# Kernel optimization log

Hardware: AMD Instinct MI355X
Metric: run time of the kernel (lower is better)

Reference implementation:

```python
import jax, jax.numpy as jnp
import numpy as np

B, T, IN_DIM = 32, 1024, 32
E, H, P = 256, 4, 32  # embed_dim, heads, max_patches
HD = E // H


def _lin(x, w, b):
    # torch nn.Linear: y = x @ W.T + b, W: [out, in]
    return jnp.einsum('...i,oi->...o', x, w) + b


def setup_inputs() -> dict:
    key = jax.random.key(0)
    ks = jax.random.split(key, 13)
    s = 0.02
    return {
        'x': jax.random.normal(ks[0], (B, T, IN_DIM), jnp.float32),
        'ip_w': jax.random.normal(ks[1], (E, IN_DIM), jnp.float32) * s,
        'ip_b': jnp.zeros((E,), jnp.float32),
        'in_proj_w': jax.random.normal(ks[2], (3 * E, E), jnp.float32) * s,
        'in_proj_b': jnp.zeros((3 * E,), jnp.float32),
        'out_w': jax.random.normal(ks[3], (E, E), jnp.float32) * s,
        'out_b': jnp.zeros((E,), jnp.float32),
        'bp_w1': jax.random.normal(ks[4], (32, E), jnp.float32) * s,
        'bp_b1': jnp.zeros((32,), jnp.float32),
        'bp_w2': jax.random.normal(ks[5], (1, 32), jnp.float32) * s,
        'bp_b2': jnp.zeros((1,), jnp.float32),
        'pr_w': jax.random.normal(ks[6], (E, E), jnp.float32) * s,
        'pr_b': jnp.zeros((E,), jnp.float32),
    }


def reference(x, ip_w, ip_b, in_proj_w, in_proj_b, out_w, out_b,
              bp_w1, bp_b1, bp_w2, bp_b2, pr_w, pr_b):
    # input projection
    h = _lin(x, ip_w, ip_b)  # [B,T,E]
    # MultiheadAttention (self-attn, batch_first, eval/no-dropout)
    qkv = _lin(h, in_proj_w, in_proj_b)  # [B,T,3E]
    q, k, v = jnp.split(qkv, 3, axis=-1)
    q = q.reshape(B, T, H, HD)
    k = k.reshape(B, T, H, HD)
    v = v.reshape(B, T, H, HD)
    scores = jnp.einsum('bqhd,bkhd->bhqk', q, k) / jnp.sqrt(jnp.float32(HD))
    attn = jax.nn.softmax(scores, axis=-1)
    ctx = jnp.einsum('bhqk,bkhd->bqhd', attn, v).reshape(B, T, E)
    attn_out = _lin(ctx, out_w, out_b)  # [B,T,E]
    # boundary scores
    bscore = jax.nn.sigmoid(_lin(jax.nn.relu(_lin(attn_out, bp_w1, bp_b1)), bp_w2, bp_b2))[..., 0]  # [B,T]
    cbp = jnp.cumsum(bscore, axis=1)
    cbp = cbp / (cbp[:, -1:] + 1e-6)
    pid = jnp.minimum(jnp.floor(cbp * P).astype(jnp.int32), P - 1)  # [B,T]
    # segment-mean pooling via scatter-add
    b_idx = jnp.broadcast_to(jnp.arange(B)[:, None], (B, T))
    pe = jnp.zeros((B, P, E), attn_out.dtype).at[b_idx, pid].add(attn_out)
    cnt = jnp.zeros((B, P), attn_out.dtype).at[b_idx, pid].add(1.0)
    pe = pe / jnp.clip(cnt, 1.0)[..., None]
    return _lin(pe, pr_w, pr_b)  # [B,P,E]
```

## Files before the change

### kernel.cpp

```cpp
#include <hip/hip_runtime.h>
#include <math.h>

constexpr int Bn  = 32;
constexpr int Tn  = 1024;
constexpr int INn = 32;
constexpr int En  = 256;
constexpr int Pn  = 32;

typedef short bf16x8 __attribute__((ext_vector_type(8)));
typedef float f32x4  __attribute__((ext_vector_type(4)));

__device__ __forceinline__ unsigned short f2bf(float f) {
    unsigned int b = __float_as_uint(f);
    b += 0x7FFF + ((b >> 16) & 1);
    return (unsigned short)(b >> 16);
}
__device__ __forceinline__ float bf2f(unsigned short h) {
    return __uint_as_float(((unsigned int)h) << 16);
}

__global__ __launch_bounds__(256) void k_prep(const float* __restrict__ ipw,
                                              const float* __restrict__ ipb,
                                              const float* __restrict__ inw,
                                              const float* __restrict__ inb,
                                              const float* __restrict__ outw,
                                              const float* __restrict__ w1,
                                              unsigned short* __restrict__ Wcb,
                                              float* __restrict__ bc,
                                              unsigned short* __restrict__ Wb,
                                              unsigned short* __restrict__ w1h,
                                              unsigned short* __restrict__ w1l) {
    int blk = blockIdx.x, tid = threadIdx.x;
    if (blk < 96) {
        int idx = blk * 256 + tid;
        int o = idx >> 5, i = idx & 31;
        const float* wr = inw + (size_t)o * En;
        float a0 = 0.f, a1 = 0.f;
        for (int e = 0; e < En; e += 2) {
            a0 += wr[e]     * ipw[(size_t)e * INn + i];
            a1 += wr[e + 1] * ipw[(size_t)(e + 1) * INn + i];
        }
        Wcb[(size_t)o * INn + i] = f2bf(a0 + a1);
    } else if (blk < 99) {
        int o = (blk - 96) * 256 + tid;
        const float* wr = inw + (size_t)o * En;
        float a = inb[o];
        for (int e = 0; e < En; ++e) a += wr[e] * ipb[e];
        bc[o] = a;
    } else if (blk < 163) {
        int idx = (blk - 99) * 256 + tid;
        float4 a = *(const float4*)(outw + (size_t)idx * 4);
        unsigned int u0 = f2bf(a.x) | ((unsigned int)f2bf(a.y) << 16);
        unsigned int u1 = f2bf(a.z) | ((unsigned int)f2bf(a.w) << 16);
        *(uint2*)(Wb + (size_t)idx * 4) = make_uint2(u0, u1);
    } else {
        int idx = (blk - 163) * 256 + tid;
        float a = w1[idx];
        unsigned short h = f2bf(a);
        w1h[idx] = h;
        w1l[idx] = f2bf(a - bf2f(h));
    }
}

__global__ __launch_bounds__(256, 2) void k_qkv(const float* __restrict__ x,
                                                const unsigned short* __restrict__ Wcb,
                                                const float* __restrict__ bc,
                                                unsigned short* __restrict__ Qb,
                                                unsigned short* __restrict__ Kb,
                                                unsigned short* __restrict__ Vt) {
    int tid = threadIdx.x;
    int wv = tid >> 6, lane = tid & 63;
    int cl = lane & 15, quad = lane >> 4;
    int m0 = blockIdx.x * 64;
    int b = m0 >> 10, tl0 = m0 & 1023;
    int n0w = wv * 192;
    f32x4 zero4 = {0.f, 0.f, 0.f, 0.f};

    bf16x8 wfrag[12]; float bv[12];
#pragma unroll
    for (int nt = 0; nt < 12; ++nt) {
        int col = n0w + nt * 16 + cl;
        wfrag[nt] = *(const bf16x8*)(Wcb + (size_t)col * 32 + quad * 8);
        bv[nt] = bc[col];
    }
#pragma unroll
    for (int mt = 0; mt < 4; ++mt) {
        const float* xr = x + (size_t)(m0 + mt * 16 + cl) * 32 + quad * 8;
        float4 xa = *(const float4*)xr, xc = *(const float4*)(xr + 4);
        bf16x8 af;
        af[0] = (short)f2bf(xa.x); af[1] = (short)f2bf(xa.y);
        af[2] = (short)f2bf(xa.z); af[3] = (short)f2bf(xa.w);
        af[4] = (short)f2bf(xc.x); af[5] = (short)f2bf(xc.y);
        af[6] = (short)f2bf(xc.z); af[7] = (short)f2bf(xc.w);
        f32x4 acc[12];
#pragma unroll
        for (int nt = 0; nt < 12; ++nt)
            acc[nt] = __builtin_amdgcn_mfma_f32_16x16x32_bf16(af, wfrag[nt], zero4, 0, 0, 0);
        int tloc = tl0 + mt * 16 + quad * 4;
#pragma unroll
        for (int nt = 0; nt < 12; ++nt) {
            int col = n0w + nt * 16 + cl;
            int slot = col >> 8, c = col & 255;
            int h = c >> 6, d = c & 63;
            int bh = b * 4 + h;
            if (slot == 2) {
                unsigned int u0 = f2bf(acc[nt][0] + bv[nt]) |
                                  ((unsigned int)f2bf(acc[nt][1] + bv[nt]) << 16);
                unsigned int u1 = f2bf(acc[nt][2] + bv[nt]) |
                                  ((unsigned int)f2bf(acc[nt][3] + bv[nt]) << 16);
                *(uint2*)(Vt + ((size_t)bh * 64 + d) * 1024 + tloc) = make_uint2(u0, u1);
            } else {
                unsigned short* dst = (slot ? Kb : Qb) +
                                      ((size_t)bh * 1024 + tloc) * 64 + d;
#pragma unroll
                for (int r = 0; r < 4; ++r)
                    dst[(size_t)r * 64] = f2bf(acc[nt][r] + bv[nt]);
            }
        }
    }
}

__global__ __launch_bounds__(256, 4) void k_attn(const unsigned short* __restrict__ Qb,
                                                 const unsigned short* __restrict__ Kb,
                                                 const unsigned short* __restrict__ Vt,
                                                 unsigned short* __restrict__ Po0,
                                                 unsigned short* __restrict__ Po1,
                                                 float* __restrict__ L0,
                                                 float* __restrict__ L1) {
    __shared__ unsigned short Ks[64][72];
    __shared__ unsigned short Vs[64][72];
    __shared__ __align__(16) unsigned short Pl[4][2][16][40];
    int blk = blockIdx.x;
    int bh = blk & 127;
    int r_ = blk >> 7;
    int qb = r_ & 7, half = r_ >> 3;
    int b = bh >> 2, h = bh & 3;
    int tid = threadIdx.x;
    int wv = tid >> 6, lane = tid & 63;
    int cl = lane & 15, quad = lane >> 4;
    int qbase = qb * 128 + wv * 32;

    f32x4 zero4 = {0.f, 0.f, 0.f, 0.f};
    bf16x8 qfrag[2][2];
#pragma unroll
    for (int tt = 0; tt < 2; ++tt)
#pragma unroll
        for (int ch = 0; ch < 2; ++ch)
            qfrag[tt][ch] = *(const bf16x8*)(Qb +
                ((size_t)bh * 1024 + qbase + tt * 16 + cl) * 64 + ch * 32 + quad * 8);
    f32x4 acc[2][4];
#pragma unroll
    for (int tt = 0; tt < 2; ++tt)
#pragma unroll
        for (int dt = 0; dt < 4; ++dt) acc[tt][dt] = zero4;
    float l[2] = {0.f, 0.f};

    const unsigned short* Kbase = Kb + (size_t)bh * 65536;
    const unsigned short* Vbase = Vt + (size_t)bh * 65536;

    for (int kt = 0; kt < 8; ++kt) {
        int ktt = half * 8 + kt;
#pragma unroll
        for (int r = 0; r < 2; ++r) {
            int idx = r * 256 + tid; int row = idx >> 3, c16 = idx & 7;
            *(uint4*)&Ks[row][c16 * 8] =
                *(const uint4*)(Kbase + (size_t)(ktt * 64 + row) * 64 + c16 * 8);
            *(uint4*)&Vs[row][c16 * 8] =
                *(const uint4*)(Vbase + (size_t)row * 1024 + ktt * 64 + c16 * 8);
        }
        __syncthreads();
#pragma unroll
        for (int c = 0; c < 2; ++c) {
            bf16x8 ka0 = *(const bf16x8*)&Ks[c * 32 + cl][quad * 8];
            bf16x8 ka1 = *(const bf16x8*)&Ks[c * 32 + cl][32 + quad * 8];
            bf16x8 kb0 = *(const bf16x8*)&Ks[c * 32 + 16 + cl][quad * 8];
            bf16x8 kb1 = *(const bf16x8*)&Ks[c * 32 + 16 + cl][32 + quad * 8];
            bf16x8 va[4];
#pragma unroll
            for (int dt = 0; dt < 4; ++dt)
                va[dt] = *(const bf16x8*)&Vs[dt * 16 + cl][c * 32 + quad * 8];
#pragma unroll
            for (int tt = 0; tt < 2; ++tt) {
                f32x4 s0 = __builtin_amdgcn_mfma_f32_16x16x32_bf16(ka0, qfrag[tt][0], zero4, 0, 0, 0);
                s0 = __builtin_amdgcn_mfma_f32_16x16x32_bf16(ka1, qfrag[tt][1], s0, 0, 0, 0);
                f32x4 s1 = __builtin_amdgcn_mfma_f32_16x16x32_bf16(kb0, qfrag[tt][0], zero4, 0, 0, 0);
                s1 = __builtin_amdgcn_mfma_f32_16x16x32_bf16(kb1, qfrag[tt][1], s1, 0, 0, 0);
                float p0 = __expf(0.125f * s0[0]), p1 = __expf(0.125f * s0[1]);
                float p2 = __expf(0.125f * s0[2]), p3 = __expf(0.125f * s0[3]);
                float p4 = __expf(0.125f * s1[0]), p5 = __expf(0.125f * s1[1]);
                float p6 = __expf(0.125f * s1[2]), p7 = __expf(0.125f * s1[3]);
                l[tt] += ((p0 + p1) + (p2 + p3)) + ((p4 + p5) + (p6 + p7));
                unsigned int w0 = f2bf(p0) | ((unsigned int)f2bf(p1) << 16);
                unsigned int w1 = f2bf(p2) | ((unsigned int)f2bf(p3) << 16);
                unsigned int w2 = f2bf(p4) | ((unsigned int)f2bf(p5) << 16);
                unsigned int w3 = f2bf(p6) | ((unsigned int)f2bf(p7) << 16);
                *(uint2*)&Pl[wv][tt][cl][quad * 4]      = make_uint2(w0, w1);
                *(uint2*)&Pl[wv][tt][cl][16 + quad * 4] = make_uint2(w2, w3);
            }
            asm volatile("s_waitcnt lgkmcnt(0)" ::: "memory");
#pragma unroll
            for (int tt = 0; tt < 2; ++tt) {
                bf16x8 pf = *(const bf16x8*)&Pl[wv][tt][cl][quad * 8];
#pragma unroll
                for (int dt = 0; dt < 4; ++dt)
                    acc[tt][dt] = __builtin_amdgcn_mfma_f32_16x16x32_bf16(pf, va[dt], acc[tt][dt], 0, 0, 0);
            }
        }
        __syncthreads();
    }
#pragma unroll
    for (int tt = 0; tt < 2; ++tt) {
        l[tt] += __shfl_xor(l[tt], 16);
        l[tt] += __shfl_xor(l[tt], 32);
    }
    unsigned short* Po = half ? Po1 : Po0;
    float* Lp = half ? L1 : L0;
#pragma unroll
    for (int tt = 0; tt < 2; ++tt) {
#pragma unroll
        for (int r = 0; r < 4; ++r) {
            size_t row = (size_t)(b * 1024 + qbase + tt * 16 + quad * 4 + r) * En;
#pragma unroll
            for (int dt = 0; dt < 4; ++dt)
                Po[row + h * 64 + dt * 16 + cl] = f2bf(acc[tt][dt][r]);
        }
    }
    if (quad == 0) {
#pragma unroll
        for (int tt = 0; tt < 2; ++tt)
            Lp[bh * 1024 + qbase + tt * 16 + cl] = l[tt];
    }
}

__global__ __launch_bounds__(256) void k_out(const unsigned short* __restrict__ Po0,
                                             const unsigned short* __restrict__ Po1,
                                             const float* __restrict__ L0,
                                             const float* __restrict__ L1,
                                             const unsigned short* __restrict__ Wb,
                                             const float* __restrict__ bias,
                                             float* __restrict__ AO) {
    __shared__ unsigned short As[64][32];
    __shared__ unsigned short Bs[256][32];
    int tid = threadIdx.x;
    int wv = tid >> 6, lane = tid & 63;
    int cl = lane & 15, quad = lane >> 4;
    size_t m0 = (size_t)blockIdx.x * 64;

    f32x4 acc[4][4];
#pragma unroll
    for (int mt = 0; mt < 4; ++mt)
#pragma unroll
        for (int nt = 0; nt < 4; ++nt) acc[mt][nt] = {0.f, 0.f, 0.f, 0.f};

    for (int kt = 0; kt < 8; ++kt) {
        if (kt) __syncthreads();
        {
            int row = tid >> 2, c4 = tid & 3;
            size_t g = (m0 + row) * En + kt * 32 + c4 * 8;
            uint4 u0 = *(const uint4*)(Po0 + g);
            uint4 u1 = *(const uint4*)(Po1 + g);
            int gt = (int)(m0 + row);
            int li = ((gt >> 10) * 4 + (kt >> 1)) * 1024 + (gt & 1023);
            float linv = 1.f / (L0[li] + L1[li]);
            unsigned int a0[4] = {u0.x, u0.y, u0.z, u0.w};
            unsigned int a1[4] = {u1.x, u1.y, u1.z, u1.w};
            unsigned int w[4];
#pragma unroll
            for (int j = 0; j < 4; ++j) {
                float lo = (bf2f((unsigned short)(a0[j] & 0xffff)) +
                            bf2f((unsigned short)(a1[j] & 0xffff))) * linv;
                float hi = (bf2f((unsigned short)(a0[j] >> 16)) +
                            bf2f((unsigned short)(a1[j] >> 16))) * linv;
                w[j] = f2bf(lo) | ((unsigned int)f2bf(hi) << 16);
            }
            *(uint4*)&As[row][c4 * 8] = make_uint4(w[0], w[1], w[2], w[3]);
        }
#pragma unroll
        for (int j = 0; j < 4; ++j) {
            int lin = j * 256 + tid; int n = lin >> 2, c = lin & 3;
            *(uint4*)&Bs[n][c * 8] =
                *(const uint4*)(Wb + (size_t)n * En + kt * 32 + c * 8);
        }
        __syncthreads();
        bf16x8 af[4], bfr[4];
#pragma unroll
        for (int mt = 0; mt < 4; ++mt)
            af[mt] = *(const bf16x8*)&As[mt * 16 + cl][quad * 8];
#pragma unroll
        for (int nt = 0; nt < 4; ++nt)
            bfr[nt] = *(const bf16x8*)&Bs[wv * 64 + nt * 16 + cl][quad * 8];
#pragma unroll
        for (int mt = 0; mt < 4; ++mt)
#pragma unroll
            for (int nt = 0; nt < 4; ++nt)
                acc[mt][nt] = __builtin_amdgcn_mfma_f32_16x16x32_bf16(af[mt], bfr[nt], acc[mt][nt], 0, 0, 0);
    }
    float bv[4];
#pragma unroll
    for (int nt = 0; nt < 4; ++nt) bv[nt] = bias[wv * 64 + nt * 16 + cl];
#pragma unroll
    for (int mt = 0; mt < 4; ++mt)
#pragma unroll
        for (int nt = 0; nt < 4; ++nt)
#pragma unroll
            for (int r = 0; r < 4; ++r)
                AO[(m0 + mt * 16 + quad * 4 + r) * En + wv * 64 + nt * 16 + cl] =
                    acc[mt][nt][r] + bv[nt];
}

__global__ __launch_bounds__(256) void k_bscore(const float* __restrict__ AO,
                                                const unsigned short* __restrict__ w1h,
                                                const unsigned short* __restrict__ w1l,
                                                const float* __restrict__ b1,
                                                const float* __restrict__ w2,
                                                const float* __restrict__ b2,
                                                float* __restrict__ bsc) {
    __shared__ unsigned short Ah[128][72];
    __shared__ unsigned short Al[128][72];
    int tid = threadIdx.x;
    int wv = tid >> 6, lane = tid & 63;
    int cl = lane & 15, quad = lane >> 4;
    int m0 = blockIdx.x * 128;

    f32x4 acc[2][2];
#pragma unroll
    for (int mt = 0; mt < 2; ++mt)
#pragma unroll
        for (int nt = 0; nt < 2; ++nt) acc[mt][nt] = {0.f, 0.f, 0.f, 0.f};

    for (int kt = 0; kt < 4; ++kt) {
        if (kt) __syncthreads();
#pragma unroll
        for (int j = 0; j < 8; ++j) {
            int lin = j * 256 + tid; int row = lin >> 4, c4 = lin & 15;
            float4 a = *(const float4*)(AO + (size_t)(m0 + row) * En + kt * 64 + c4 * 4);
            unsigned short h0 = f2bf(a.x), h1v = f2bf(a.y), h2 = f2bf(a.z), h3 = f2bf(a.w);
            unsigned short l0 = f2bf(a.x - bf2f(h0)), l1v = f2bf(a.y - bf2f(h1v));
            unsigned short l2 = f2bf(a.z - bf2f(h2)), l3 = f2bf(a.w - bf2f(h3));
            *(uint2*)&Ah[row][c4 * 4] =
                make_uint2(h0 | ((unsigned int)h1v << 16), h2 | ((unsigned int)h3 << 16));
            *(uint2*)&Al[row][c4 * 4] =
                make_uint2(l0 | ((unsigned int)l1v << 16), l2 | ((unsigned int)l3 << 16));
        }
        __syncthreads();
#pragma unroll
        for (int ks = 0; ks < 2; ++ks) {
            bf16x8 bh_[2], bl_[2];
#pragma unroll
            for (int nt = 0; nt < 2; ++nt) {
                size_t off = (size_t)(nt * 16 + cl) * En + kt * 64 + ks * 32 + quad * 8;
                bh_[nt] = *(const bf16x8*)(w1h + off);
                bl_[nt] = *(const bf16x8*)(w1l + off);
            }
#pragma unroll
            for (int mt = 0; mt < 2; ++mt) {
                int row = wv * 32 + mt * 16 + cl;
                bf16x8 ah = *(const bf16x8*)&Ah[row][ks * 32 + quad * 8];
                bf16x8 al = *(const bf16x8*)&Al[row][ks * 32 + quad * 8];
#pragma unroll
                for (int nt = 0; nt < 2; ++nt) {
                    acc[mt][nt] = __builtin_amdgcn_mfma_f32_16x16x32_bf16(ah, bh_[nt], acc[mt][nt], 0, 0, 0);
                    acc[mt][nt] = __builtin_amdgcn_mfma_f32_16x16x32_bf16(ah, bl_[nt], acc[mt][nt], 0, 0, 0);
                    acc[mt][nt] = __builtin_amdgcn_mfma_f32_16x16x32_bf16(al, bh_[nt], acc[mt][nt], 0, 0, 0);
                }
            }
        }
    }
    float b1v[2], w2v[2];
#pragma unroll
    for (int nt = 0; nt < 2; ++nt) {
        b1v[nt] = b1[nt * 16 + cl];
        w2v[nt] = w2[nt * 16 + cl];
    }
    float b2v = b2[0];
#pragma unroll
    for (int mt = 0; mt < 2; ++mt) {
        f32x4 z;
#pragma unroll
        for (int r = 0; r < 4; ++r)
            z[r] = fmaxf(acc[mt][0][r] + b1v[0], 0.f) * w2v[0] +
                   fmaxf(acc[mt][1][r] + b1v[1], 0.f) * w2v[1];
#pragma unroll
        for (int d = 1; d < 16; d <<= 1)
#pragma unroll
            for (int r = 0; r < 4; ++r) z[r] += __shfl_xor(z[r], d);
        if (cl == 0) {
#pragma unroll
            for (int r = 0; r < 4; ++r)
                bsc[m0 + wv * 32 + mt * 16 + quad * 4 + r] =
                    1.f / (1.f + __expf(-(z[r] + b2v)));
        }
    }
}

__global__ __launch_bounds__(1024) void k_scan(const float* __restrict__ bsc,
                                               int* __restrict__ segs) {
    __shared__ float wsum[16];
    __shared__ float s_pre[1024];
    __shared__ float s_tot;
    int b = blockIdx.x, t = threadIdx.x;
    float x = bsc[b * Tn + t];
#pragma unroll
    for (int d = 1; d < 64; d <<= 1) {
        float y = __shfl_up(x, d);
        if ((t & 63) >= d) x += y;
    }
    int w = t >> 6;
    if ((t & 63) == 63) wsum[w] = x;
    __syncthreads();
    if (t == 0) {
        float s = 0.f;
        for (int i = 0; i < 16; ++i) { float tmp = wsum[i]; wsum[i] = s; s += tmp; }
        s_tot = s;
    }
    __syncthreads();
    float pre = x + wsum[w];
    s_pre[t] = pre;
    __syncthreads();
    float denom = s_tot + 1e-6f;
    float qv = pre / denom * 32.0f;
    int pid = min((int)floorf(qv), 31);
    int pidprev = -1;
    if (t > 0) {
        float qp = s_pre[t - 1] / denom * 32.0f;
        pidprev = min((int)floorf(qp), 31);
    }
    for (int p = pidprev + 1; p <= pid; ++p) segs[b * 33 + p] = t;
    if (t == 1023)
        for (int p = pid + 1; p <= 32; ++p) segs[b * 33 + p] = Tn;
}

__global__ __launch_bounds__(256) void k_pool_proj(const float* __restrict__ ao,
                                                   const int* __restrict__ segs,
                                                   const float* __restrict__ prw,
                                                   const float* __restrict__ prb,
                                                   float* __restrict__ out) {
    __shared__ float pes[En];
    int b = blockIdx.y, p = blockIdx.x;
    int s = segs[b * 33 + p];
    int e = segs[b * 33 + p + 1];
    int tid = threadIdx.x;
    float sum = 0.f;
    for (int t = s; t < e; ++t)
        sum += ao[((size_t)b * Tn + t) * En + tid];
    pes[tid] = sum / fmaxf((float)(e - s), 1.f);
    __syncthreads();
    float a0 = prb[tid], a1 = 0.f;
#pragma unroll
    for (int k = 0; k < En; k += 4) {
        float4 wv = *(const float4*)(prw + (size_t)tid * En + k);
        float4 pv = *(const float4*)&pes[k];
        a0 += wv.x * pv.x; a1 += wv.y * pv.y;
        a0 += wv.z * pv.z; a1 += wv.w * pv.w;
    }
    out[((size_t)b * Pn + p) * En + tid] = a0 + a1;
}

extern "C" void kernel_launch(void* const* d_in, const int* in_sizes, int n_in,
                              void* d_out, int out_size, void* d_ws, size_t ws_size,
                              hipStream_t stream) {
    const float* x    = (const float*)d_in[0];
    const float* ipw  = (const float*)d_in[1];
    const float* ipb  = (const float*)d_in[2];
    const float* inw  = (const float*)d_in[3];
    const float* inb  = (const float*)d_in[4];
    const float* outw = (const float*)d_in[5];
    const float* outb = (const float*)d_in[6];
    const float* bw1  = (const float*)d_in[7];
    const float* bb1  = (const float*)d_in[8];
    const float* bw2  = (const float*)d_in[9];
    const float* bb2  = (const float*)d_in[10];
    const float* prw  = (const float*)d_in[11];
    const float* prb  = (const float*)d_in[12];

    char* base = (char*)d_ws;
    unsigned short* Qb  = (unsigned short*)base;
    unsigned short* Kb  = Qb + (size_t)8388608;
    float*          AO  = (float*)base;
    unsigned short* Vt  = (unsigned short*)(base + (size_t)33554432);
    unsigned short* Po0 = (unsigned short*)(base + (size_t)50331648);
    unsigned short* Po1 = (unsigned short*)(base + (size_t)67108864);
    unsigned short* Wcb = (unsigned short*)(base + (size_t)83886080);
    float*          bc  = (float*)(base + (size_t)83935232);
    unsigned short* Wb  = (unsigned short*)(base + (size_t)83938304);
    unsigned short* w1h = (unsigned short*)(base + (size_t)84069376);
    unsigned short* w1l = (unsigned short*)(base + (size_t)84085760);
    float*          L0  = (float*)(base + (size_t)84102144);
    float*          L1  = (float*)(base + (size_t)84626432);
    float*          bsc = (float*)(base + (size_t)85150720);
    int*           segs = (int*)(base + (size_t)85281792);

    k_prep<<<195, 256, 0, stream>>>(ipw, ipb, inw, inb, outw, bw1,
                                    Wcb, bc, Wb, w1h, w1l);
    k_qkv<<<512, 256, 0, stream>>>(x, Wcb, bc, Qb, Kb, Vt);
    k_attn<<<2048, 256, 0, stream>>>(Qb, Kb, Vt, Po0, Po1, L0, L1);
    k_out<<<512, 256, 0, stream>>>(Po0, Po1, L0, L1, Wb, outb, AO);
    k_bscore<<<256, 256, 0, stream>>>(AO, w1h, w1l, bb1, bw2, bb2, bsc);
    k_scan<<<32, 1024, 0, stream>>>(bsc, segs);
    k_pool_proj<<<dim3(32, 32), 256, 0, stream>>>(AO, segs, prw, prb,
                                                  (float*)d_out);
}
```

Measured before the change: 237.8 us.

## Fuse scan with pooling projection, enlarge attention tiles, move weight casts into qkv

```diff
diff --git a/kernel.cpp b/kernel.cpp
--- a/kernel.cpp
+++ b/kernel.cpp
@@ -18,18 +18,17 @@
 __device__ __forceinline__ float bf2f(unsigned short h) {
     return __uint_as_float(((unsigned int)h) << 16);
 }
+__device__ __forceinline__ unsigned int permpack(float lo, float hi) {
+    return __builtin_amdgcn_perm(__float_as_uint(hi), __float_as_uint(lo),
+                                 0x07060302u);
+}
 
 __global__ __launch_bounds__(256) void k_prep(const float* __restrict__ ipw,
                                               const float* __restrict__ ipb,
                                               const float* __restrict__ inw,
                                               const float* __restrict__ inb,
-                                              const float* __restrict__ outw,
-                                              const float* __restrict__ w1,
                                               unsigned short* __restrict__ Wcb,
-                                              float* __restrict__ bc,
-                                              unsigned short* __restrict__ Wb,
-                                              unsigned short* __restrict__ w1h,
-                                              unsigned short* __restrict__ w1l) {
+                                              float* __restrict__ bc) {
     int blk = blockIdx.x, tid = threadIdx.x;
     if (blk < 96) {
         int idx = blk * 256 + tid;
@@ -41,34 +40,53 @@
             a1 += wr[e + 1] * ipw[(size_t)(e + 1) * INn + i];
         }
         Wcb[(size_t)o * INn + i] = f2bf(a0 + a1);
-    } else if (blk < 99) {
+    } else {
         int o = (blk - 96) * 256 + tid;
         const float* wr = inw + (size_t)o * En;
         float a = inb[o];
         for (int e = 0; e < En; ++e) a += wr[e] * ipb[e];
         bc[o] = a;
-    } else if (blk < 163) {
-        int idx = (blk - 99) * 256 + tid;
-        float4 a = *(const float4*)(outw + (size_t)idx * 4);
-        unsigned int u0 = f2bf(a.x) | ((unsigned int)f2bf(a.y) << 16);
-        unsigned int u1 = f2bf(a.z) | ((unsigned int)f2bf(a.w) << 16);
-        *(uint2*)(Wb + (size_t)idx * 4) = make_uint2(u0, u1);
-    } else {
-        int idx = (blk - 163) * 256 + tid;
-        float a = w1[idx];
-        unsigned short h = f2bf(a);
-        w1h[idx] = h;
-        w1l[idx] = f2bf(a - bf2f(h));
     }
 }
 
 __global__ __launch_bounds__(256, 2) void k_qkv(const float* __restrict__ x,
                                                 const unsigned short* __restrict__ Wcb,
                                                 const float* __restrict__ bc,
+                                                const float* __restrict__ outw,
+                                                const float* __restrict__ w1,
+                                                const float* __restrict__ prw,
                                                 unsigned short* __restrict__ Qb,
                                                 unsigned short* __restrict__ Kb,
-                                                unsigned short* __restrict__ Vt) {
+                                                unsigned short* __restrict__ Vt,
+                                                unsigned short* __restrict__ Wb,
+                                                unsigned short* __restrict__ w1h,
+                                                unsigned short* __restrict__ w1l,
+                                                unsigned short* __restrict__ pwh,
+                                                unsigned short* __restrict__ pwl) {
     int tid = threadIdx.x;
+    if (blockIdx.x >= 512) {
+        int cb = blockIdx.x - 512;
+        if (cb < 64) {
+            int idx = cb * 256 + tid;
+            float4 a = *(const float4*)(outw + (size_t)idx * 4);
+            unsigned int u0 = f2bf(a.x) | ((unsigned int)f2bf(a.y) << 16);
+            unsigned int u1 = f2bf(a.z) | ((unsigned int)f2bf(a.w) << 16);
+            *(uint2*)(Wb + (size_t)idx * 4) = make_uint2(u0, u1);
+        } else if (cb < 96) {
+            int idx = (cb - 64) * 256 + tid;
+            float a = w1[idx];
+            unsigned short h = f2bf(a);
+            w1h[idx] = h;
+            w1l[idx] = f2bf(a - bf2f(h));
+        } else {
+            int idx = (cb - 96) * 256 + tid;
+            float a = prw[idx];
+            unsigned short h = f2bf(a);
+            pwh[idx] = h;
+            pwl[idx] = f2bf(a - bf2f(h));
+        }
+        return;
+    }
     int wv = tid >> 6, lane = tid & 63;
     int cl = lane & 15, quad = lane >> 4;
     int m0 = blockIdx.x * 64;
@@ -129,31 +147,32 @@
                                                  float* __restrict__ L1) {
     __shared__ unsigned short Ks[64][72];
     __shared__ unsigned short Vs[64][72];
-    __shared__ __align__(16) unsigned short Pl[4][2][16][40];
+    __shared__ __align__(16) unsigned short Pl[4][4][16][40];
     int blk = blockIdx.x;
     int bh = blk & 127;
     int r_ = blk >> 7;
-    int qb = r_ & 7, half = r_ >> 3;
+    int qb = r_ & 3, half = r_ >> 2;
     int b = bh >> 2, h = bh & 3;
     int tid = threadIdx.x;
     int wv = tid >> 6, lane = tid & 63;
     int cl = lane & 15, quad = lane >> 4;
-    int qbase = qb * 128 + wv * 32;
+    int qbase = qb * 256 + wv * 64;
+    const float SCL = 0.18033688f;
 
     f32x4 zero4 = {0.f, 0.f, 0.f, 0.f};
-    bf16x8 qfrag[2][2];
-#pragma unroll
-    for (int tt = 0; tt < 2; ++tt)
+    bf16x8 qfrag[4][2];
+#pragma unroll
+    for (int tt = 0; tt < 4; ++tt)
 #pragma unroll
         for (int ch = 0; ch < 2; ++ch)
             qfrag[tt][ch] = *(const bf16x8*)(Qb +
                 ((size_t)bh * 1024 + qbase + tt * 16 + cl) * 64 + ch * 32 + quad * 8);
-    f32x4 acc[2][4];
-#pragma unroll
-    for (int tt = 0; tt < 2; ++tt)
+    f32x4 acc[4][4];
+#pragma unroll
+    for (int tt = 0; tt < 4; ++tt)
 #pragma unroll
         for (int dt = 0; dt < 4; ++dt) acc[tt][dt] = zero4;
-    float l[2] = {0.f, 0.f};
+    float l[4] = {0.f, 0.f, 0.f, 0.f};
 
     const unsigned short* Kbase = Kb + (size_t)bh * 65536;
     const unsigned short* Vbase = Vt + (size_t)bh * 65536;
@@ -180,26 +199,29 @@
             for (int dt = 0; dt < 4; ++dt)
                 va[dt] = *(const bf16x8*)&Vs[dt * 16 + cl][c * 32 + quad * 8];
 #pragma unroll
-            for (int tt = 0; tt < 2; ++tt) {
+            for (int tt = 0; tt < 4; ++tt) {
                 f32x4 s0 = __builtin_amdgcn_mfma_f32_16x16x32_bf16(ka0, qfrag[tt][0], zero4, 0, 0, 0);
                 s0 = __builtin_amdgcn_mfma_f32_16x16x32_bf16(ka1, qfrag[tt][1], s0, 0, 0, 0);
                 f32x4 s1 = __builtin_amdgcn_mfma_f32_16x16x32_bf16(kb0, qfrag[tt][0], zero4, 0, 0, 0);
                 s1 = __builtin_amdgcn_mfma_f32_16x16x32_bf16(kb1, qfrag[tt][1], s1, 0, 0, 0);
-                float p0 = __expf(0.125f * s0[0]), p1 = __expf(0.125f * s0[1]);
-                float p2 = __expf(0.125f * s0[2]), p3 = __expf(0.125f * s0[3]);
-                float p4 = __expf(0.125f * s1[0]), p5 = __expf(0.125f * s1[1]);
-                float p6 = __expf(0.125f * s1[2]), p7 = __expf(0.125f * s1[3]);
-                l[tt] += ((p0 + p1) + (p2 + p3)) + ((p4 + p5) + (p6 + p7));
-                unsigned int w0 = f2bf(p0) | ((unsigned int)f2bf(p1) << 16);
-                unsigned int w1 = f2bf(p2) | ((unsigned int)f2bf(p3) << 16);
-                unsigned int w2 = f2bf(p4) | ((unsigned int)f2bf(p5) << 16);
-                unsigned int w3 = f2bf(p6) | ((unsigned int)f2bf(p7) << 16);
+                float p0 = exp2f(SCL * s0[0]), p1 = exp2f(SCL * s0[1]);
+                float p2 = exp2f(SCL * s0[2]), p3 = exp2f(SCL * s0[3]);
+                float p4 = exp2f(SCL * s1[0]), p5 = exp2f(SCL * s1[1]);
+                float p6 = exp2f(SCL * s1[2]), p7 = exp2f(SCL * s1[3]);
+                unsigned int w0 = permpack(p0, p1);
+                unsigned int w1 = permpack(p2, p3);
+                unsigned int w2 = permpack(p4, p5);
+                unsigned int w3 = permpack(p6, p7);
+                l[tt] += ((__uint_as_float(w0 << 16) + __uint_as_float(w0 & 0xffff0000u)) +
+                          (__uint_as_float(w1 << 16) + __uint_as_float(w1 & 0xffff0000u))) +
+                         ((__uint_as_float(w2 << 16) + __uint_as_float(w2 & 0xffff0000u)) +
+                          (__uint_as_float(w3 << 16) + __uint_as_float(w3 & 0xffff0000u)));
                 *(uint2*)&Pl[wv][tt][cl][quad * 4]      = make_uint2(w0, w1);
                 *(uint2*)&Pl[wv][tt][cl][16 + quad * 4] = make_uint2(w2, w3);
             }
             asm volatile("s_waitcnt lgkmcnt(0)" ::: "memory");
 #pragma unroll
-            for (int tt = 0; tt < 2; ++tt) {
+            for (int tt = 0; tt < 4; ++tt) {
                 bf16x8 pf = *(const bf16x8*)&Pl[wv][tt][cl][quad * 8];
 #pragma unroll
                 for (int dt = 0; dt < 4; ++dt)
@@ -209,14 +231,14 @@
         __syncthreads();
     }
 #pragma unroll
-    for (int tt = 0; tt < 2; ++tt) {
+    for (int tt = 0; tt < 4; ++tt) {
         l[tt] += __shfl_xor(l[tt], 16);
         l[tt] += __shfl_xor(l[tt], 32);
     }
     unsigned short* Po = half ? Po1 : Po0;
     float* Lp = half ? L1 : L0;
 #pragma unroll
-    for (int tt = 0; tt < 2; ++tt) {
+    for (int tt = 0; tt < 4; ++tt) {
 #pragma unroll
         for (int r = 0; r < 4; ++r) {
             size_t row = (size_t)(b * 1024 + qbase + tt * 16 + quad * 4 + r) * En;
@@ -227,7 +249,7 @@
     }
     if (quad == 0) {
 #pragma unroll
-        for (int tt = 0; tt < 2; ++tt)
+        for (int tt = 0; tt < 4; ++tt)
             Lp[bh * 1024 + qbase + tt * 16 + cl] = l[tt];
     }
 }
@@ -393,11 +415,18 @@
     }
 }
 
-__global__ __launch_bounds__(1024) void k_scan(const float* __restrict__ bsc,
-                                               int* __restrict__ segs) {
+__global__ __launch_bounds__(1024) void k_tail(const float* __restrict__ bsc,
+                                               const float* __restrict__ AO,
+                                               const unsigned short* __restrict__ pwh,
+                                               const unsigned short* __restrict__ pwl,
+                                               const float* __restrict__ prb,
+                                               float* __restrict__ out) {
+    __shared__ float s_pre[1024];
     __shared__ float wsum[16];
-    __shared__ float s_pre[1024];
     __shared__ float s_tot;
+    __shared__ int   segs[33];
+    __shared__ unsigned short PEh[32][264];
+    __shared__ unsigned short PEl[32][264];
     int b = blockIdx.x, t = threadIdx.x;
     float x = bsc[b * Tn + t];
 #pragma unroll
@@ -418,42 +447,54 @@
     s_pre[t] = pre;
     __syncthreads();
     float denom = s_tot + 1e-6f;
-    float qv = pre / denom * 32.0f;
-    int pid = min((int)floorf(qv), 31);
+    int pid = min((int)floorf(pre / denom * 32.0f), 31);
     int pidprev = -1;
-    if (t > 0) {
-        float qp = s_pre[t - 1] / denom * 32.0f;
-        pidprev = min((int)floorf(qp), 31);
-    }
-    for (int p = pidprev + 1; p <= pid; ++p) segs[b * 33 + p] = t;
+    if (t > 0) pidprev = min((int)floorf(s_pre[t - 1] / denom * 32.0f), 31);
+    for (int p = pidprev + 1; p <= pid; ++p) segs[p] = t;
     if (t == 1023)
-        for (int p = pid + 1; p <= 32; ++p) segs[b * 33 + p] = Tn;
-}
-
-__global__ __launch_bounds__(256) void k_pool_proj(const float* __restrict__ ao,
-                                                   const int* __restrict__ segs,
-                                                   const float* __restrict__ prw,
-                                                   const float* __restrict__ prb,
-                                                   float* __restrict__ out) {
-    __shared__ float pes[En];
-    int b = blockIdx.y, p = blockIdx.x;
-    int s = segs[b * 33 + p];
-    int e = segs[b * 33 + p + 1];
-    int tid = threadIdx.x;
-    float sum = 0.f;
-    for (int t = s; t < e; ++t)
-        sum += ao[((size_t)b * Tn + t) * En + tid];
-    pes[tid] = sum / fmaxf((float)(e - s), 1.f);
+        for (int p = pid + 1; p <= 32; ++p) segs[p] = Tn;
     __syncthreads();
-    float a0 = prb[tid], a1 = 0.f;
-#pragma unroll
-    for (int k = 0; k < En; k += 4) {
-        float4 wv = *(const float4*)(prw + (size_t)tid * En + k);
-        float4 pv = *(const float4*)&pes[k];
-        a0 += wv.x * pv.x; a1 += wv.y * pv.y;
-        a0 += wv.z * pv.z; a1 += wv.w * pv.w;
-    }
-    out[((size_t)b * Pn + p) * En + tid] = a0 + a1;
+    {
+        int g = t >> 8, e = t & 255;
+#pragma unroll
+        for (int i = 0; i < 8; ++i) {
+            int p = g * 8 + i;
+            int s = segs[p], en = segs[p + 1];
+            float sum = 0.f;
+            for (int tk = s; tk < en; ++tk)
+                sum += AO[((size_t)b * Tn + tk) * En + e];
+            float mean = sum / fmaxf((float)(en - s), 1.f);
+            unsigned short hh = f2bf(mean);
+            PEh[p][e] = hh;
+            PEl[p][e] = f2bf(mean - bf2f(hh));
+        }
+    }
+    __syncthreads();
+    {
+        int wv = t >> 6, lane = t & 63;
+        int cl = lane & 15, quad = lane >> 4;
+        int n = wv * 16 + cl;
+        f32x4 acc[2] = {{0.f, 0.f, 0.f, 0.f}, {0.f, 0.f, 0.f, 0.f}};
+        for (int kt = 0; kt < 8; ++kt) {
+            bf16x8 bh_ = *(const bf16x8*)(pwh + (size_t)n * En + kt * 32 + quad * 8);
+            bf16x8 bl_ = *(const bf16x8*)(pwl + (size_t)n * En + kt * 32 + quad * 8);
+#pragma unroll
+            for (int mt = 0; mt < 2; ++mt) {
+                bf16x8 ah = *(const bf16x8*)&PEh[mt * 16 + cl][kt * 32 + quad * 8];
+                bf16x8 al = *(const bf16x8*)&PEl[mt * 16 + cl][kt * 32 + quad * 8];
+                acc[mt] = __builtin_amdgcn_mfma_f32_16x16x32_bf16(ah, bh_, acc[mt], 0, 0, 0);
+                acc[mt] = __builtin_amdgcn_mfma_f32_16x16x32_bf16(ah, bl_, acc[mt], 0, 0, 0);
+                acc[mt] = __builtin_amdgcn_mfma_f32_16x16x32_bf16(al, bh_, acc[mt], 0, 0, 0);
+            }
+        }
+        float bv = prb[n];
+#pragma unroll
+        for (int mt = 0; mt < 2; ++mt)
+#pragma unroll
+            for (int r = 0; r < 4; ++r)
+                out[(size_t)(b * Pn + mt * 16 + quad * 4 + r) * En + n] =
+                    acc[mt][r] + bv;
+    }
 }
 
 extern "C" void kernel_launch(void* const* d_in, const int* in_sizes, int n_in,
@@ -488,15 +529,14 @@
     float*          L0  = (float*)(base + (size_t)84102144);
     float*          L1  = (float*)(base + (size_t)84626432);
     float*          bsc = (float*)(base + (size_t)85150720);
-    int*           segs = (int*)(base + (size_t)85281792);
-
-    k_prep<<<195, 256, 0, stream>>>(ipw, ipb, inw, inb, outw, bw1,
-                                    Wcb, bc, Wb, w1h, w1l);
-    k_qkv<<<512, 256, 0, stream>>>(x, Wcb, bc, Qb, Kb, Vt);
-    k_attn<<<2048, 256, 0, stream>>>(Qb, Kb, Vt, Po0, Po1, L0, L1);
+    unsigned short* pwh = (unsigned short*)(base + (size_t)85286912);
+    unsigned short* pwl = (unsigned short*)(base + (size_t)85417984);
+
+    k_prep<<<99, 256, 0, stream>>>(ipw, ipb, inw, inb, Wcb, bc);
+    k_qkv<<<864, 256, 0, stream>>>(x, Wcb, bc, outw, bw1, prw,
+                                   Qb, Kb, Vt, Wb, w1h, w1l, pwh, pwl);
+    k_attn<<<1024, 256, 0, stream>>>(Qb, Kb, Vt, Po0, Po1, L0, L1);
     k_out<<<512, 256, 0, stream>>>(Po0, Po1, L0, L1, Wb, outb, AO);
     k_bscore<<<256, 256, 0, stream>>>(AO, w1h, w1l, bb1, bw2, bb2, bsc);
-    k_scan<<<32, 1024, 0, stream>>>(bsc, segs);
-    k_pool_proj<<<dim3(32, 32), 256, 0, stream>>>(AO, segs, prw, prb,
-                                                  (float*)d_out);
-}
+    k_tail<<<32, 1024, 0, stream>>>(bsc, AO, pwh, pwl, prb, (float*)d_out);
+}
```

After: 426.3 us. 79.3% more time.
